# Optimization experiments

Measured on AMD Instinct MI355X. Metric: run time of the kernel, lower is better.

The kernel has to match this reference:

```python
import jax, jax.numpy as jnp
import numpy as np

IN, HID, B = 512, 512, 16384

def _linear_params(key, fan_in, fan_out, bias_const=None):
    kw, kb = jax.random.split(key)
    bound = 1.0 / np.sqrt(fan_in)
    W = jax.random.uniform(kw, (fan_out, fan_in), jnp.float32, -bound, bound)
    if bias_const is None:
        b = jax.random.uniform(kb, (fan_out,), jnp.float32, -bound, bound)
    else:
        b = jnp.full((fan_out,), bias_const, jnp.float32)
    return W, b

def setup_inputs() -> dict:
    key = jax.random.key(0)
    ks = jax.random.split(key, 11)
    x = jax.random.normal(ks[0], (B, IN), jnp.float32)
    h = jax.random.normal(ks[1], (B, HID), jnp.float32)
    c = jax.random.normal(ks[2], (B, HID), jnp.float32)
    Wxi, bxi = _linear_params(ks[3], IN, HID)
    Wxo, bxo = _linear_params(ks[4], IN, HID)
    Wxf, bxf = _linear_params(ks[5], IN, HID, bias_const=1.0)
    Wxg, bxg = _linear_params(ks[6], IN, HID)
    Whi, bhi = _linear_params(ks[7], HID, HID)
    Who, bho = _linear_params(ks[8], HID, HID)
    Whf, bhf = _linear_params(ks[9], HID, HID, bias_const=1.0)
    Whg, bhg = _linear_params(ks[10], HID, HID)
    return dict(x=x, h=h, c=c,
                Wxi=Wxi, bxi=bxi, Wxo=Wxo, bxo=bxo, Wxf=Wxf, bxf=bxf, Wxg=Wxg, bxg=bxg,
                Whi=Whi, bhi=bhi, Who=Who, bho=bho, Whf=Whf, bhf=bhf, Whg=Whg, bhg=bhg)

def reference(x, h, c,
              Wxi, bxi, Wxo, bxo, Wxf, bxf, Wxg, bxg,
              Whi, bhi, Who, bho, Whf, bhf, Whg, bhg):
    # Batch the four input projections and four hidden projections into two GEMMs.
    Wx = jnp.concatenate([Wxi, Wxg, Wxf, Wxo], axis=0)   # [4H, IN]
    Wh = jnp.concatenate([Whi, Whg, Whf, Who], axis=0)   # [4H, HID]
    bx = jnp.concatenate([bxi, bxg, bxf, bxo], axis=0)
    bh = jnp.concatenate([bhi, bhg, bhf, bho], axis=0)
    gates = x @ Wx.T + h @ Wh.T + bx + bh                 # [B, 4H]
    i_pre, g_pre, f_pre, o_pre = jnp.split(gates, 4, axis=1)
    i = jax.nn.sigmoid(i_pre)
    g = jnp.tanh(g_pre)
    f = jax.nn.sigmoid(f_pre)
    o = jax.nn.sigmoid(o_pre)
    c_new = f * c + i * g
    h_new = o * jnp.tanh(c_new)
    return (h_new, c_new)
```

## Files before the change

### kernel.cpp

```cpp
#include <hip/hip_runtime.h>
#include <cstdint>
#include <cstddef>


#define BATCH 16384
#define KDIM  1024
#define NPK   2048
#define HIDN  512
#define NKT   32

typedef __bf16 bf16x8 __attribute__((ext_vector_type(8)));
typedef float  f32x4  __attribute__((ext_vector_type(4)));

__device__ __forceinline__ unsigned short f2bf(float f) {
  unsigned int u = __builtin_bit_cast(unsigned int, f);
  u += 0x7fffu + ((u >> 16) & 1u);
  return (unsigned short)(u >> 16);
}

__device__ __forceinline__ float fast_sigmoid(float x) {
  return __builtin_amdgcn_rcpf(1.0f + __expf(-x));
}
__device__ __forceinline__ float fast_tanh(float x) {
  return 1.0f - 2.0f * __builtin_amdgcn_rcpf(1.0f + __expf(2.0f * x));
}

__global__ __launch_bounds__(256) void pack_a2(const float* __restrict__ x,
                                               const float* __restrict__ h,
                                               unsigned short* __restrict__ A) {
  int c = blockIdx.x * 256 + threadIdx.x;
  int lane = c & 63;
  int g    = (c >> 6) & 7;
  int kt   = (c >> 9) & 31;
  int bm   = c >> 14;
  int row  = bm * 128 + g * 16 + (lane & 15);
  int col  = kt * 32 + ((lane >> 4) << 3);
  const float* src = (col < 512) ? (x + (size_t)row * 512 + col)
                                 : (h + (size_t)row * 512 + (col - 512));
  float4 lo = ((const float4*)src)[0];
  float4 hi = ((const float4*)src)[1];
  union { unsigned short s[8]; uint4 u; } o;
  o.s[0]=f2bf(lo.x); o.s[1]=f2bf(lo.y); o.s[2]=f2bf(lo.z); o.s[3]=f2bf(lo.w);
  o.s[4]=f2bf(hi.x); o.s[5]=f2bf(hi.y); o.s[6]=f2bf(hi.z); o.s[7]=f2bf(hi.w);
  ((uint4*)A)[c] = o.u;
}

struct GatePtrs {
  const float* wx[4];
  const float* wh[4];
  const float* bx[4];
  const float* bh[4];
};

__global__ __launch_bounds__(256) void pack_w2(GatePtrs P,
                                               unsigned short* __restrict__ W,
                                               float* __restrict__ bias) {
  int c = blockIdx.x * 256 + threadIdx.x;
  int lane = c & 63;
  int ni   = (c >> 6) & 3;
  int wn   = (c >> 8) & 1;
  int kt   = (c >> 9) & 31;
  int bn   = c >> 14;
  int jl   = lane & 15;
  int j    = bn * 32 + wn * 16 + jl;
  int col  = kt * 32 + ((lane >> 4) << 3);
  const float* src = (col < 512) ? (P.wx[ni] + (size_t)j * 512 + col)
                                 : (P.wh[ni] + (size_t)j * 512 + (col - 512));
  float4 lo = ((const float4*)src)[0];
  float4 hi = ((const float4*)src)[1];
  union { unsigned short s[8]; uint4 u; } o;
  o.s[0]=f2bf(lo.x); o.s[1]=f2bf(lo.y); o.s[2]=f2bf(lo.z); o.s[3]=f2bf(lo.w);
  o.s[4]=f2bf(hi.x); o.s[5]=f2bf(hi.y); o.s[6]=f2bf(hi.z); o.s[7]=f2bf(hi.w);
  ((uint4*)W)[c] = o.u;
  if (kt == 0 && (lane >> 4) == 0)
    bias[bn * 128 + wn * 64 + ni * 16 + jl] = P.bx[ni][j] + P.bh[ni][j];
}


__global__ __launch_bounds__(256) void lstm_gemm(
    const bf16x8* __restrict__ Af,
    const bf16x8* __restrict__ Bf,
    const float* __restrict__ bias,
    const float* __restrict__ Cin,
    float* __restrict__ Hout,
    float* __restrict__ Cout) {
  const int tid  = threadIdx.x;
  const int lane = tid & 63;
  const int wv   = tid >> 6;
  const int wm   = wv >> 1;
  const int wn   = wv & 1;
  const int bn   = blockIdx.x;
  const int bm   = blockIdx.y;

  const bf16x8* pa = Af + ((size_t)bm * 256 + wm * 4) * 64 + lane;
  const bf16x8* pb = Bf + ((size_t)bn * 256 + wn * 4) * 64 + lane;

  f32x4 acc[4][4] = {};
  bf16x8 fa[2][4], fb[2][4];

#pragma unroll
  for (int i = 0; i < 4; ++i) { fa[0][i] = pa[i * 64]; fb[0][i] = pb[i * 64]; }

#pragma unroll
  for (int kt = 0; kt < NKT; ++kt) {
    const int cur = kt & 1;
    if (kt + 1 < NKT) {
      const bf16x8* qa = pa + (kt + 1) * 512;
      const bf16x8* qb = pb + (kt + 1) * 512;
#pragma unroll
      for (int i = 0; i < 4; ++i) {
        fa[cur ^ 1][i] = qa[i * 64];
        fb[cur ^ 1][i] = qb[i * 64];
      }
    }
#pragma unroll
    for (int mi = 0; mi < 4; ++mi)
#pragma unroll
      for (int ni = 0; ni < 4; ++ni)
        acc[mi][ni] = __builtin_amdgcn_mfma_f32_16x16x32_bf16(
            fa[cur][mi], fb[cur][ni], acc[mi][ni], 0, 0, 0);
  }

  const int jl = lane & 15;
  const int j  = bn * 32 + wn * 16 + jl;
  const int rbase = bm * 128 + wm * 64 + ((lane >> 4) << 2);
  float bv[4];
#pragma unroll
  for (int ni = 0; ni < 4; ++ni)
    bv[ni] = bias[bn * 128 + wn * 64 + ni * 16 + jl];

#pragma unroll
  for (int mi = 0; mi < 4; ++mi) {
#pragma unroll
    for (int r = 0; r < 4; ++r) {
      int row = rbase + mi * 16 + r;
      float iv = fast_sigmoid(acc[mi][0][r] + bv[0]);
      float gv = fast_tanh   (acc[mi][1][r] + bv[1]);
      float fv = fast_sigmoid(acc[mi][2][r] + bv[2]);
      float ov = fast_sigmoid(acc[mi][3][r] + bv[3]);
      float cold = Cin[(size_t)row * HIDN + j];
      float cnew = fv * cold + iv * gv;
      Hout[(size_t)row * HIDN + j] = ov * fast_tanh(cnew);
      Cout[(size_t)row * HIDN + j] = cnew;
    }
  }
}


extern "C" void kernel_launch(void* const* d_in, const int* in_sizes, int n_in,
                              void* d_out, int out_size, void* d_ws, size_t ws_size,
                              hipStream_t stream) {
  const float* x   = (const float*)d_in[0];
  const float* h   = (const float*)d_in[1];
  const float* c   = (const float*)d_in[2];
  const float* Wxi = (const float*)d_in[3];  const float* bxi = (const float*)d_in[4];
  const float* Wxo = (const float*)d_in[5];  const float* bxo = (const float*)d_in[6];
  const float* Wxf = (const float*)d_in[7];  const float* bxf = (const float*)d_in[8];
  const float* Wxg = (const float*)d_in[9];  const float* bxg = (const float*)d_in[10];
  const float* Whi = (const float*)d_in[11]; const float* bhi = (const float*)d_in[12];
  const float* Who = (const float*)d_in[13]; const float* bho = (const float*)d_in[14];
  const float* Whf = (const float*)d_in[15]; const float* bhf = (const float*)d_in[16];
  const float* Whg = (const float*)d_in[17]; const float* bhg = (const float*)d_in[18];

  char* ws = (char*)d_ws;
  unsigned short* Apack = (unsigned short*)ws;
  unsigned short* Wpack = (unsigned short*)(ws + (size_t)BATCH * KDIM * 2);
  float* biasp = (float*)(ws + (size_t)BATCH * KDIM * 2 + (size_t)NPK * KDIM * 2);

  pack_a2<<<(BATCH * KDIM / 8) / 256, 256, 0, stream>>>(x, h, Apack);

  GatePtrs P;
  P.wx[0] = Wxi; P.wx[1] = Wxg; P.wx[2] = Wxf; P.wx[3] = Wxo;
  P.wh[0] = Whi; P.wh[1] = Whg; P.wh[2] = Whf; P.wh[3] = Who;
  P.bx[0] = bxi; P.bx[1] = bxg; P.bx[2] = bxf; P.bx[3] = bxo;
  P.bh[0] = bhi; P.bh[1] = bhg; P.bh[2] = bhf; P.bh[3] = bho;
  pack_w2<<<(NPK * KDIM / 8) / 256, 256, 0, stream>>>(P, Wpack, biasp);

  float* Hout = (float*)d_out;
  float* Cout = Hout + (size_t)BATCH * HIDN;
  dim3 grid(NPK / 128, BATCH / 128);
  lstm_gemm<<<grid, 256, 0, stream>>>((const bf16x8*)Apack, (const bf16x8*)Wpack,
                                      biasp, c, Hout, Cout);
}
```

Measured before the change: 284.3 us.

## Remap GEMM blocks per XCD for L2 reuse and deepen register prefetch

The 2D grid becomes a 1D grid of 2048 blocks. Each block's linear index is decoded so that consecutive blocks, which are dispatched round-robin across the 8 XCDs, share the same M-tile within an XCD. All 16 N-tiles of a given A row-block then run on one XCD, so that XCD's L2 serves the A reuse. The register prefetch also goes from double to triple buffering, loading two k-steps ahead to hide global-load latency. The extra buffer costs more VGPRs and may lower occupancy.

```diff
diff --git a/kernel.cpp b/kernel.cpp
--- a/kernel.cpp
+++ b/kernel.cpp
@@ -89,28 +89,39 @@
   const int wv   = tid >> 6;
   const int wm   = wv >> 1;
   const int wn   = wv & 1;
-  const int bn   = blockIdx.x;
-  const int bm   = blockIdx.y;
+
+  const int lin = blockIdx.x;
+  const int xcd = lin & 7;
+  const int idx = lin >> 3;
+  const int bn  = idx & 15;
+  const int bmi = idx >> 4;
+  const int bm  = bmi * 8 + xcd;
 
   const bf16x8* pa = Af + ((size_t)bm * 256 + wm * 4) * 64 + lane;
   const bf16x8* pb = Bf + ((size_t)bn * 256 + wn * 4) * 64 + lane;
 
   f32x4 acc[4][4] = {};
-  bf16x8 fa[2][4], fb[2][4];
+  bf16x8 fa[3][4], fb[3][4];
 
 #pragma unroll
-  for (int i = 0; i < 4; ++i) { fa[0][i] = pa[i * 64]; fb[0][i] = pb[i * 64]; }
+  for (int p = 0; p < 2; ++p) {
+    const bf16x8* qa = pa + (size_t)p * 512;
+    const bf16x8* qb = pb + (size_t)p * 512;
+#pragma unroll
+    for (int i = 0; i < 4; ++i) { fa[p][i] = qa[i * 64]; fb[p][i] = qb[i * 64]; }
+  }
 
 #pragma unroll
   for (int kt = 0; kt < NKT; ++kt) {
-    const int cur = kt & 1;
-    if (kt + 1 < NKT) {
-      const bf16x8* qa = pa + (kt + 1) * 512;
-      const bf16x8* qb = pb + (kt + 1) * 512;
+    const int cur = kt % 3;
+    if (kt + 2 < NKT) {
+      const int nxt = (kt + 2) % 3;
+      const bf16x8* qa = pa + (size_t)(kt + 2) * 512;
+      const bf16x8* qb = pb + (size_t)(kt + 2) * 512;
 #pragma unroll
       for (int i = 0; i < 4; ++i) {
-        fa[cur ^ 1][i] = qa[i * 64];
-        fb[cur ^ 1][i] = qb[i * 64];
+        fa[nxt][i] = qa[i * 64];
+        fb[nxt][i] = qb[i * 64];
       }
     }
 #pragma unroll
@@ -178,7 +189,7 @@
 
   float* Hout = (float*)d_out;
   float* Cout = Hout + (size_t)BATCH * HIDN;
-  dim3 grid(NPK / 128, BATCH / 128);
-  lstm_gemm<<<grid, 256, 0, stream>>>((const bf16x8*)Apack, (const bf16x8*)Wpack,
-                                      biasp, c, Hout, Cout);
+  lstm_gemm<<<dim3(2048), 256, 0, stream>>>((const bf16x8*)Apack,
+                                            (const bf16x8*)Wpack,
+                                            biasp, c, Hout, Cout);
 }
```

Measured after the change: 276.7 us. -2.7%, faster.
